# Optimization experiments

Hardware: AMD Instinct MI355X
Metric: run time of the kernel (lower is better)

Reference implementation:

```python
import jax, jax.numpy as jnp
import numpy as np

K = 3
PAD = 1
STRIDE = 1
DIL = 1


def _conv_offset(x, w, b):
    # standard 3x3 conv, NCHW
    out = jax.lax.conv_general_dilated(
        x, w, window_strides=(STRIDE, STRIDE), padding=((PAD, PAD), (PAD, PAD)),
        rhs_dilation=(DIL, DIL), dimension_numbers=('NCHW', 'OIHW', 'NCHW'))
    return out + b[None, :, None, None]


def _bilinear_sample(x, px, py):
    # x: (b,c,h,w); px,py: (b,N) absolute pixel coords; zero padding outside.
    b, c, h, w = x.shape
    x_flat = x.reshape(b, c, h * w)
    x0 = jnp.floor(px)
    y0 = jnp.floor(py)
    wx1 = px - x0
    wy1 = py - y0
    wx0 = 1.0 - wx1
    wy0 = 1.0 - wy1

    def gather(xi, yi, wt):
        valid = (xi >= 0) & (xi <= w - 1) & (yi >= 0) & (yi <= h - 1)
        xc = jnp.clip(xi, 0, w - 1).astype(jnp.int32)
        yc = jnp.clip(yi, 0, h - 1).astype(jnp.int32)
        idx = yc * w + xc  # (b,N)
        v = jax.vmap(lambda xf, i: jnp.take(xf, i, axis=1))(x_flat, idx)  # (b,c,N)
        return v * (wt * valid.astype(x.dtype))[:, None, :]

    out = gather(x0, y0, wy0 * wx0)
    out = out + gather(x0 + 1, y0, wy0 * wx1)
    out = out + gather(x0, y0 + 1, wy1 * wx0)
    out = out + gather(x0 + 1, y0 + 1, wy1 * wx1)
    return out


def setup_inputs() -> dict:
    key = jax.random.key(0)
    k1, k2, k3, k4 = jax.random.split(key, 4)
    x = jax.random.normal(k1, (8, 64, 128, 128), dtype=jnp.float32)
    # small random offset-predictor weights (repo inits to zero; random gives nonzero offsets)
    w_off = jax.random.normal(k2, (27, 64, 3, 3), dtype=jnp.float32) * 0.01
    b_off = jax.random.normal(k3, (27,), dtype=jnp.float32) * 0.01
    w_conv = jax.random.normal(k4, (64, 576), dtype=jnp.float32) / np.sqrt(3.0 * 576.0)
    return {"x": x, "w_off": w_off, "b_off": b_off, "w_conv": w_conv}


def reference(x, w_off, b_off, w_conv):
    b, c, h, w = x.shape
    out = _conv_offset(x, w_off, b_off)  # (b, 3*K*K, H, W)
    H, W = out.shape[2], out.shape[3]
    o1, o2, m = jnp.split(out, 3, axis=1)  # each (b, K*K, H, W)
    mask = jax.nn.sigmoid(m).reshape(b, 1, K, K, H, W)
    # base grid (absolute coords), per module __init__
    x_start = DIL / 2 * (K - 1) - PAD  # = 0.0 here
    y_start = DIL / 2 * (K - 1) - PAD
    x_cood = (x_start + STRIDE * jnp.arange(W)).astype(x.dtype)
    y_cood = (y_start + STRIDE * jnp.arange(H)).astype(x.dtype)
    # per-tap kernel bias, tap order is (kh, kw) row-major
    taps = (jnp.arange(K) - (K - 1) / 2) * DIL
    x_bias = jnp.tile(taps, K).astype(x.dtype)      # (K*K,)
    y_bias = jnp.repeat(taps, K).astype(x.dtype)    # (K*K,)
    px = o1 + x_cood[None, None, None, :] + x_bias[None, :, None, None]  # (b,9,H,W)
    py = o2 + y_cood[None, None, :, None] + y_bias[None, :, None, None]
    N = K * K * H * W
    y = _bilinear_sample(x, px.reshape(b, N), py.reshape(b, N))  # (b,c,N)
    y = y.reshape(b, c, K, K, H, W) * mask
    y = y.reshape(b, c * K * K, H, W)
    # 1x1 conv == channel GEMM
    return jnp.einsum('bkhw,ok->bohw', y, w_conv)
```

## Files before the change

kernel.cpp:

```cpp
#include <hip/hip_runtime.h>
#include <math.h>

#define HW_   128
#define CIN_  64
#define IMG_  (HW_ * HW_)

#define TR_    6
#define TC_    40
#define PIT_   36
#define TILEDW (TR_ * TC_ * PIT_)

typedef short    s16x8 __attribute__((ext_vector_type(8)));
typedef float    f32x4 __attribute__((ext_vector_type(4)));
typedef unsigned u32x4 __attribute__((ext_vector_type(4)));

__device__ __forceinline__ short f2bf(float f) {
  union { float f; unsigned i; } v; v.f = f;
  unsigned r = (v.i + 0x7fffu + ((v.i >> 16) & 1u)) >> 16;
  return (short)r;
}

#if defined(__has_builtin)
#if __has_builtin(__builtin_amdgcn_cvt_pk_bf16_f32)
#define HAVE_CVT_PK_BF16 1
#endif
#endif

__device__ __forceinline__ unsigned PK2(float a, float b) {
#ifdef HAVE_CVT_PK_BF16
  typedef __bf16 bf16x2_t __attribute__((ext_vector_type(2)));
  union { bf16x2_t v; unsigned u; } cv;
  cv.v = __builtin_amdgcn_cvt_pk_bf16_f32(a, b);
  return cv.u;
#else
  union { float f; unsigned u; } ua, ub; ua.f = a; ub.f = b;
  unsigned ra = ua.u + 0x7fffu + ((ua.u >> 16) & 1u);
  unsigned rb = ub.u + 0x7fffu + ((ub.u >> 16) & 1u);
  return __builtin_amdgcn_perm(rb, ra, 0x07060302u);
#endif
}

__device__ __forceinline__ float bfl(unsigned d) {
  union { unsigned u; float f; } v; v.u = d << 16; return v.f;
}
__device__ __forceinline__ float bfh(unsigned d) {
  union { unsigned u; float f; } v; v.u = d; return v.f;
}


__global__ __launch_bounds__(256) void wprep(const float* __restrict__ w_off,
                                             const float* __restrict__ w_conv,
                                             short* __restrict__ wOf,
                                             short* __restrict__ wA) {
  int t = blockIdx.x * 256 + threadIdx.x;
  if (t < 36864) {
    int i = t & 7, o = (t >> 3) & 63, q = (t >> 9) & 3, ks = (t >> 11) & 1, j = t >> 12;
    int c = ks * 32 + q * 8 + i;
    wA[t] = f2bf(w_conv[o * 576 + c * 9 + j]);
  }
  if (t < 18432) {
    int i = t & 7, m = (t >> 3) & 31, q = (t >> 8) & 3, ks = (t >> 10) & 1, j = t >> 11;
    int c = ks * 32 + q * 8 + i;
    wOf[t] = (m < 27) ? f2bf(w_off[(m * 64 + c) * 9 + j]) : (short)0;
  }
}

__global__ __launch_bounds__(256)
__attribute__((amdgpu_waves_per_eu(4)))
void dfuse(const float* __restrict__ x,
           const short* __restrict__ wOf,
           const float* __restrict__ b_off,
           const short* __restrict__ wA,
           float* __restrict__ out) {
  __shared__ __align__(16) unsigned lds_[TILEDW];

  int bi  = blockIdx.x >> 8;
  int tid = blockIdx.x & 255;
  int h0  = (tid >> 2) << 1;
  int w0  = (tid & 3) << 5;
  int t   = threadIdx.x;
  int wv  = t >> 6, l = t & 63;
  int col = l & 15, q = l >> 4;
  int px_local = wv * 16 + col;
  int rl  = px_local >> 5;
  int cl  = px_local & 31;
  int h   = h0 + rl;
  int w   = w0 + cl;
  int p   = h * HW_ + w;

  const float* xB = x + (size_t)bi * (CIN_ * IMG_);

  for (int u = t; u < TR_ * 32 * 10; u += 256) {
    int cc = u % 10;
    int rc = u / 10;
    int cp = rc & 31;
    int r  = rc >> 5;
    int y  = h0 - 2 + r;
    int ys = min(max(y, 0), HW_ - 1);
    int xg0 = w0 - 4 + cc * 4;
    int xs  = min(max(xg0, 0), HW_ - 4);
    bool ok = (y >= 0) && (y < HW_) && (xg0 >= 0) && (xg0 < HW_);
    const float* s0 = xB + (2 * cp) * IMG_ + ys * HW_ + xs;
    float4 f0 = *(const float4*)s0;
    float4 f1 = *(const float4*)(s0 + IMG_);
    int sd = (r * TC_ + cc * 4) * PIT_ + cp;
    lds_[sd]            = ok ? PK2(f0.x, f1.x) : 0u;
    lds_[sd + PIT_]     = ok ? PK2(f0.y, f1.y) : 0u;
    lds_[sd + 2 * PIT_] = ok ? PK2(f0.z, f1.z) : 0u;
    lds_[sd + 3 * PIT_] = ok ? PK2(f0.w, f1.w) : 0u;
  }
  __syncthreads();

  float oall[32];
  {
    const short* wq = wOf + q * 256 + col * 8;
    f32x4 a0v = {0.f, 0.f, 0.f, 0.f};
    f32x4 a1v = {0.f, 0.f, 0.f, 0.f};
    const unsigned* tb = &lds_[((rl + 2) * TC_ + (cl + 4)) * PIT_ + q * 4];
#pragma unroll
    for (int j = 0; j < 9; ++j) {
      int dy = j / 3 - 1, dx = j % 3 - 1;
      const unsigned* tp = tb + (dy * TC_ + dx) * PIT_;
      union { u32x4 u; s16x8 v; } B0, B1;
      B0.u = *(const u32x4*)tp;
      B1.u = *(const u32x4*)(tp + 16);
      const short* wj = wq + j * 2048;
      s16x8 a00 = *(const s16x8*)(wj);
      s16x8 a01 = *(const s16x8*)(wj + 128);
      s16x8 a10 = *(const s16x8*)(wj + 1024);
      s16x8 a11 = *(const s16x8*)(wj + 1024 + 128);
      a0v = __builtin_amdgcn_mfma_f32_16x16x32_bf16(a00, B0.v, a0v, 0, 0, 0);
      a1v = __builtin_amdgcn_mfma_f32_16x16x32_bf16(a01, B0.v, a1v, 0, 0, 0);
      a0v = __builtin_amdgcn_mfma_f32_16x16x32_bf16(a10, B1.v, a0v, 0, 0, 0);
      a1v = __builtin_amdgcn_mfma_f32_16x16x32_bf16(a11, B1.v, a1v, 0, 0, 0);
    }
    float myv[8];
#pragma unroll
    for (int r = 0; r < 4; ++r) myv[r] = a0v[r] + b_off[q * 4 + r];
#pragma unroll
    for (int r = 0; r < 4; ++r) {
      int ch = 16 + q * 4 + r;
      float bo = b_off[min(ch, 26)];
      float v = a1v[r] + bo;
      myv[4 + r] = (ch >= 18) ? (1.f / (1.f + __expf(-v))) : v;
    }
#pragma unroll
    for (int qq = 0; qq < 4; ++qq) {
      int src = qq * 16 + col;
#pragma unroll
      for (int r = 0; r < 4; ++r) {
        oall[qq * 4 + r]      = __shfl(myv[r], src);
        oall[16 + qq * 4 + r] = __shfl(myv[4 + r], src);
      }
    }
  }

  f32x4 acc[4];
#pragma unroll
  for (int ms = 0; ms < 4; ++ms) acc[ms] = (f32x4){0.f, 0.f, 0.f, 0.f};

  const short* wqA = wA + q * 512 + col * 8;

#pragma unroll
  for (int j = 0; j < 9; ++j) {
    float o1 = oall[j], o2 = oall[9 + j], mk = oall[18 + j];

    float pxf = o1 + (float)(w + (j % 3) - 1);
    float pyf = o2 + (float)(h + (j / 3) - 1);
    float fx = floorf(pxf), fy = floorf(pyf);
    int   x0 = (int)fx,   y0 = (int)fy;
    float ax = pxf - fx, ay = pyf - fy;
    float bx = 1.f - ax, by = 1.f - ay;

    bx = (x0 >= 0  && x0 < HW_)     ? bx : 0.f;
    ax = (x0 >= -1 && x0 < HW_ - 1) ? ax : 0.f;
    by = (y0 >= 0  && y0 < HW_)     ? by : 0.f;
    ay = (y0 >= -1 && y0 < HW_ - 1) ? ay : 0.f;
    float bym = by * mk, aym = ay * mk;
    float u00 = bym * bx, u01 = bym * ax;
    float u10 = aym * bx, u11 = aym * ax;

    unsigned F0u[4], F1u[4];
    bool intile = (o1 >= -1.f) && (o1 < 1.f) && (o2 >= -1.f) && (o2 < 1.f);
    if (intile) {
      int r0 = y0 - (h0 - 2), c0 = x0 - (w0 - 4);
      const unsigned* t00 = &lds_[(r0 * TC_ + c0) * PIT_ + q * 4];
      u32x4 A00 = *(const u32x4*)(t00);
      u32x4 A01 = *(const u32x4*)(t00 + PIT_);
      u32x4 A10 = *(const u32x4*)(t00 + TC_ * PIT_);
      u32x4 A11 = *(const u32x4*)(t00 + TC_ * PIT_ + PIT_);
      u32x4 B00 = *(const u32x4*)(t00 + 16);
      u32x4 B01 = *(const u32x4*)(t00 + PIT_ + 16);
      u32x4 B10 = *(const u32x4*)(t00 + TC_ * PIT_ + 16);
      u32x4 B11 = *(const u32x4*)(t00 + TC_ * PIT_ + PIT_ + 16);
#pragma unroll
      for (int i = 0; i < 4; ++i) {
        float vlo = fmaf(bfl(A00[i]), u00, fmaf(bfl(A01[i]), u01,
                    fmaf(bfl(A10[i]), u10, bfl(A11[i]) * u11)));
        float vhi = fmaf(bfh(A00[i]), u00, fmaf(bfh(A01[i]), u01,
                    fmaf(bfh(A10[i]), u10, bfh(A11[i]) * u11)));
        F0u[i] = PK2(vlo, vhi);
        float wlo = fmaf(bfl(B00[i]), u00, fmaf(bfl(B01[i]), u01,
                    fmaf(bfl(B10[i]), u10, bfl(B11[i]) * u11)));
        float whi = fmaf(bfh(B00[i]), u00, fmaf(bfh(B01[i]), u01,
                    fmaf(bfh(B10[i]), u10, bfh(B11[i]) * u11)));
        F1u[i] = PK2(wlo, whi);
      }
    } else {
      int xc0 = min(max(x0, 0), HW_ - 1), xc1 = min(max(x0 + 1, 0), HW_ - 1);
      int yc0 = min(max(y0, 0), HW_ - 1), yc1 = min(max(y0 + 1, 0), HW_ - 1);
      int g00 = yc0 * HW_ + xc0, g01 = yc0 * HW_ + xc1;
      int g10 = yc1 * HW_ + xc0, g11 = yc1 * HW_ + xc1;
      for (int hB = 0; hB < 2; ++hB) {
        for (int ii = 0; ii < 4; ++ii) {
          int c0i = hB * 32 + q * 8 + 2 * ii;
          const float* pc = xB + c0i * IMG_;
          const float* pd = pc + IMG_;
          float va = u00 * pc[g00] + u01 * pc[g01] + u10 * pc[g10] + u11 * pc[g11];
          float vb = u00 * pd[g00] + u01 * pd[g01] + u10 * pd[g10] + u11 * pd[g11];
          if (hB) F1u[ii] = PK2(va, vb); else F0u[ii] = PK2(va, vb);
        }
      }
    }

    union { unsigned u[4]; s16x8 v; } F0, F1;
#pragma unroll
    for (int i = 0; i < 4; ++i) { F0.u[i] = F0u[i]; F1.u[i] = F1u[i]; }

    const short* wj = wqA + j * 4096;
#pragma unroll
    for (int ms = 0; ms < 4; ++ms) {
      s16x8 a0 = *(const s16x8*)(wj + ms * 128);
      acc[ms] = __builtin_amdgcn_mfma_f32_16x16x32_bf16(a0, F0.v, acc[ms], 0, 0, 0);
    }
#pragma unroll
    for (int ms = 0; ms < 4; ++ms) {
      s16x8 a1 = *(const s16x8*)(wj + 2048 + ms * 128);
      acc[ms] = __builtin_amdgcn_mfma_f32_16x16x32_bf16(a1, F1.v, acc[ms], 0, 0, 0);
    }
  }

  float* op = out + (size_t)bi * (CIN_ * IMG_) + p;
#pragma unroll
  for (int ms = 0; ms < 4; ++ms)
#pragma unroll
    for (int r = 0; r < 4; ++r)
      op[(ms * 16 + q * 4 + r) * IMG_] = acc[ms][r];
}

extern "C" void kernel_launch(void* const* d_in, const int* in_sizes, int n_in,
                              void* d_out, int out_size, void* d_ws, size_t ws_size,
                              hipStream_t stream) {
  const float* x      = (const float*)d_in[0];
  const float* w_off  = (const float*)d_in[1];
  const float* b_off  = (const float*)d_in[2];
  const float* w_conv = (const float*)d_in[3];
  float* out = (float*)d_out;

  char* ws = (char*)d_ws;
  short* wOf = (short*)(ws);
  short* wA  = (short*)(ws + 36864);

  hipLaunchKernelGGL(wprep, dim3(144),  dim3(256), 0, stream, w_off, w_conv, wOf, wA);
  hipLaunchKernelGGL(dfuse, dim3(2048), dim3(256), 0, stream, x, wOf, b_off, wA, out);
}
```

Measured before the change: 142.2 us.

## Pack bilinear interpolation into float2 ops and interleave batches across blocks

Measured after the change: 127.9 us. 10.0% less time.

```diff
diff --git a/kernel.cpp b/kernel.cpp
--- a/kernel.cpp
+++ b/kernel.cpp
@@ -12,6 +12,7 @@
 
 typedef short    s16x8 __attribute__((ext_vector_type(8)));
 typedef float    f32x4 __attribute__((ext_vector_type(4)));
+typedef float    f32x2 __attribute__((ext_vector_type(2)));
 typedef unsigned u32x4 __attribute__((ext_vector_type(4)));
 
 __device__ __forceinline__ short f2bf(float f) {
@@ -40,11 +41,10 @@
 #endif
 }
 
-__device__ __forceinline__ float bfl(unsigned d) {
-  union { unsigned u; float f; } v; v.u = d << 16; return v.f;
-}
-__device__ __forceinline__ float bfh(unsigned d) {
-  union { unsigned u; float f; } v; v.u = d; return v.f;
+__device__ __forceinline__ f32x2 up2d(unsigned d) {
+  union { unsigned u; float f; } lo, hi;
+  lo.u = d << 16; hi.u = d;
+  return (f32x2){lo.f, hi.f};
 }
 
 
@@ -74,8 +74,8 @@
            float* __restrict__ out) {
   __shared__ __align__(16) unsigned lds_[TILEDW];
 
-  int bi  = blockIdx.x >> 8;
-  int tid = blockIdx.x & 255;
+  int bi  = blockIdx.x & 7;
+  int tid = blockIdx.x >> 3;
   int h0  = (tid >> 2) << 1;
   int w0  = (tid & 3) << 5;
   int t   = threadIdx.x;
@@ -179,6 +179,8 @@
     float bym = by * mk, aym = ay * mk;
     float u00 = bym * bx, u01 = bym * ax;
     float u10 = aym * bx, u11 = aym * ax;
+    f32x2 U00 = {u00, u00}, U01 = {u01, u01};
+    f32x2 U10 = {u10, u10}, U11 = {u11, u11};
 
     unsigned F0u[4], F1u[4];
     bool intile = (o1 >= -1.f) && (o1 < 1.f) && (o2 >= -1.f) && (o2 < 1.f);
@@ -195,16 +197,12 @@
       u32x4 B11 = *(const u32x4*)(t00 + TC_ * PIT_ + PIT_ + 16);
 #pragma unroll
       for (int i = 0; i < 4; ++i) {
-        float vlo = fmaf(bfl(A00[i]), u00, fmaf(bfl(A01[i]), u01,
-                    fmaf(bfl(A10[i]), u10, bfl(A11[i]) * u11)));
-        float vhi = fmaf(bfh(A00[i]), u00, fmaf(bfh(A01[i]), u01,
-                    fmaf(bfh(A10[i]), u10, bfh(A11[i]) * u11)));
-        F0u[i] = PK2(vlo, vhi);
-        float wlo = fmaf(bfl(B00[i]), u00, fmaf(bfl(B01[i]), u01,
-                    fmaf(bfl(B10[i]), u10, bfl(B11[i]) * u11)));
-        float whi = fmaf(bfh(B00[i]), u00, fmaf(bfh(B01[i]), u01,
-                    fmaf(bfh(B10[i]), u10, bfh(B11[i]) * u11)));
-        F1u[i] = PK2(wlo, whi);
+        f32x2 v0 = up2d(A00[i]) * U00 + up2d(A01[i]) * U01
+                 + up2d(A10[i]) * U10 + up2d(A11[i]) * U11;
+        F0u[i] = PK2(v0.x, v0.y);
+        f32x2 v1 = up2d(B00[i]) * U00 + up2d(B01[i]) * U01
+                 + up2d(B10[i]) * U10 + up2d(B11[i]) * U11;
+        F1u[i] = PK2(v1.x, v1.y);
       }
     } else {
       int xc0 = min(max(x0, 0), HW_ - 1), xc1 = min(max(x0 + 1, 0), HW_ - 1);
```
